# Optimization experiments

Measured on AMD Instinct MI355X. Metric: run time of the kernel, lower is better.

The kernel has to match this reference:

```python
import jax, jax.numpy as jnp
import numpy as np

N = 50000
E = 500000
D = 128
L = 3
BN_EPS = 1e-5


def setup_inputs() -> dict:
    key = jax.random.key(0)
    ks = jax.random.split(key, 16)

    def xavier(k, shape):
        fan_in, fan_out = shape[-2], shape[-1]
        limit = float(np.sqrt(6.0 / (fan_in + fan_out)))
        return jax.random.uniform(k, shape, jnp.float32, -limit, limit)

    inp = {
        "x": jax.random.randint(ks[0], (N, 2), 0, 3),
        "edge_index": jax.random.randint(ks[1], (2, E), 0, N),
        "edge_attr": jax.random.randint(ks[2], (E, 2), 0, 3),
        # atom embeddings (xavier_uniform like torch init)
        "atom_emb0": xavier(ks[3], (120, D)),
        "atom_emb1": xavier(ks[4], (3, D)),
        # per-layer edge embeddings, stacked over layers
        "edge_emb0": xavier(ks[5], (L, 5, D)),
        "edge_emb1": xavier(ks[6], (L, 3, D)),
        # per-layer MLP: Linear(D, 2D) -> ReLU -> Linear(2D, D)
        "W1": xavier(ks[7], (L, D, 2 * D)),
        "b1": jnp.zeros((L, 2 * D), jnp.float32),
        "W2": xavier(ks[8], (L, 2 * D, D)),
        "b2": jnp.zeros((L, D), jnp.float32),
        # batchnorm affine params
        "gamma": jnp.ones((L, D), jnp.float32),
        "beta": jnp.zeros((L, D), jnp.float32),
    }
    return inp


def reference(x, edge_index, edge_attr, atom_emb0, atom_emb1,
              edge_emb0, edge_emb1, W1, b1, W2, b2, gamma, beta):
    n = x.shape[0]
    num_layer = W1.shape[0]

    # atom embedding: sum of per-attribute embeddings -> [N, D]
    h = atom_emb0[x[:, 0]] + atom_emb1[x[:, 1]]

    # add self loops: src/dst both get arange(N) appended
    loop = jnp.arange(n, dtype=edge_index.dtype)
    src = jnp.concatenate([edge_index[0], loop])  # [E+N]
    dst = jnp.concatenate([edge_index[1], loop])  # [E+N]
    # self-loop edge attr is [4, 0]
    ea0 = jnp.concatenate([edge_attr[:, 0], jnp.full((n,), 4, edge_attr.dtype)])
    ea1 = jnp.concatenate([edge_attr[:, 1], jnp.zeros((n,), edge_attr.dtype)])

    for l in range(num_layer):
        # edge embedding lookup + message = x_j + edge_attr, scatter-add to dst
        eemb = edge_emb0[l][ea0] + edge_emb1[l][ea1]          # [E+N, D]
        msg = h[src] + eemb                                   # gather + add
        aggr = jax.ops.segment_sum(msg, dst, num_segments=n)  # [N, D]
        # MLP update
        hid = jax.nn.relu(aggr @ W1[l] + b1[l])               # [N, 2D]
        out = hid @ W2[l] + b2[l]                             # [N, D]
        # BatchNorm1d (training mode: batch stats, biased variance)
        mean = jnp.mean(out, axis=0)
        var = jnp.mean(jnp.square(out - mean), axis=0)
        out = gamma[l] * (out - mean) * jax.lax.rsqrt(var + BN_EPS) + beta[l]
        # dropout with p=0 is identity; ReLU on all but last layer
        h = out if l == num_layer - 1 else jax.nn.relu(out)
    return h
```

## Files before the change

kernel.cpp:

```cpp
#include <hip/hip_runtime.h>

#define D 128
#define TWO_D 256
#define BN_EPS 1e-5f

typedef __attribute__((ext_vector_type(8))) short bf16x8;
typedef __attribute__((ext_vector_type(4))) float f32x4;

__device__ __forceinline__ float relu_f(float x) { return x > 0.f ? x : 0.f; }

__device__ __forceinline__ unsigned short f2bf(float f) {
    unsigned u = __builtin_bit_cast(unsigned, f);
    return (unsigned short)((u + 0x7FFFu + ((u >> 16) & 1u)) >> 16);
}
__device__ __forceinline__ float bf2f(unsigned s) {
    unsigned u = s << 16;
    return __builtin_bit_cast(float, u);
}
__device__ __forceinline__ unsigned pack2(float a, float b) {
    return (unsigned)f2bf(a) | ((unsigned)f2bf(b) << 16);
}

__global__ void atom_embed_kernel(const int* __restrict__ x,
                                  const float* __restrict__ emb0,
                                  const float* __restrict__ emb1,
                                  unsigned short* __restrict__ hbf, int n) {
    int idx = blockIdx.x * blockDim.x + threadIdx.x;
    if (idx >= n * 32) return;
    int node = idx >> 5;
    int d0 = (idx & 31) << 2;
    int i0 = x[node * 2 + 0];
    int i1 = x[node * 2 + 1];
    const float4 a = *reinterpret_cast<const float4*>(emb0 + (size_t)i0 * D + d0);
    const float4 b = *reinterpret_cast<const float4*>(emb1 + (size_t)i1 * D + d0);
    uint2 v;
    v.x = pack2(a.x + b.x, a.y + b.y);
    v.y = pack2(a.z + b.z, a.w + b.w);
    *reinterpret_cast<uint2*>(hbf + (size_t)node * D + d0) = v;
}

__global__ void hist_kernel(const int* __restrict__ ei, int* __restrict__ counts, int e_cnt) {
    int e = blockIdx.x * blockDim.x + threadIdx.x;
    if (e >= e_cnt) return;
    atomicAdd(counts + ei[e_cnt + e], 1);
}

__global__ __launch_bounds__(256) void bsum_kernel(const int* __restrict__ counts,
                                                   int* __restrict__ bsum, int n) {
    __shared__ int s[256];
    int t = threadIdx.x;
    int idx = blockIdx.x * 256 + t;
    s[t] = (idx < n) ? counts[idx] : 0;
    __syncthreads();
    for (int off = 128; off > 0; off >>= 1) {
        if (t < off) s[t] += s[t + off];
        __syncthreads();
    }
    if (t == 0) bsum[blockIdx.x] = s[0];
}

__global__ __launch_bounds__(256) void bscan_kernel(const int* __restrict__ bsum,
                                                    int* __restrict__ bpre,
                                                    int* __restrict__ row_ptr, int nb, int n) {
    __shared__ int s[256];
    int t = threadIdx.x;
    s[t] = (t < nb) ? bsum[t] : 0;
    __syncthreads();
    for (int off = 1; off < 256; off <<= 1) {
        int v = (t >= off) ? s[t - off] : 0;
        __syncthreads();
        s[t] += v;
        __syncthreads();
    }
    bpre[t] = (t == 0) ? 0 : s[t - 1];
    if (t == 255) row_ptr[n] = s[255];
}

__global__ __launch_bounds__(256) void scan_apply_kernel(const int* __restrict__ counts,
                                                         const int* __restrict__ bpre,
                                                         int* __restrict__ row_ptr,
                                                         int* __restrict__ cursor, int n) {
    __shared__ int s[256];
    int t = threadIdx.x;
    int idx = blockIdx.x * 256 + t;
    int c = (idx < n) ? counts[idx] : 0;
    s[t] = c;
    __syncthreads();
    for (int off = 1; off < 256; off <<= 1) {
        int v = (t >= off) ? s[t - off] : 0;
        __syncthreads();
        s[t] += v;
        __syncthreads();
    }
    if (idx < n) {
        int excl = bpre[blockIdx.x] + s[t] - c;
        row_ptr[idx] = excl;
        cursor[idx] = excl;
    }
}

__global__ void fill_kernel(const int* __restrict__ ei, const int* __restrict__ ea,
                            int* __restrict__ cursor, int* __restrict__ epack, int e_cnt) {
    int e = blockIdx.x * blockDim.x + threadIdx.x;
    if (e >= e_cnt) return;
    int dst = ei[e_cnt + e];
    int src = ei[e];
    int aidx = ea[e * 2 + 0] * 3 + ea[e * 2 + 1];
    int pos = atomicAdd(cursor + dst, 1);
    epack[pos] = (src & 0x1FFFF) | (aidx << 17);
}

__global__ void frag_prep_kernel(const float* __restrict__ W1,
                                 const float* __restrict__ W2,
                                 unsigned short* __restrict__ w1f,
                                 unsigned short* __restrict__ w2f, int Lnum) {
    int tid = blockIdx.x * blockDim.x + threadIdx.x;
    if (tid >= Lnum * 128 * 64) return;
    int l = tid / 8192;
    int rem = tid % 8192;
    int frag = rem / 64;
    int lane = rem % 64;
    int kg = lane >> 4, cl = lane & 15;
    if (frag < 64) {
        int kk = frag >> 4, tn = frag & 15;
        const float* src = W1 + (size_t)l * D * TWO_D;
        int k0 = kk * 32 + kg * 8, col = tn * 16 + cl;
        unsigned short* dst = w1f + (size_t)l * 32768 + ((size_t)frag * 64 + lane) * 8;
        #pragma unroll
        for (int j = 0; j < 8; ++j) dst[j] = f2bf(src[(size_t)(k0 + j) * TWO_D + col]);
    } else {
        int f2 = frag - 64;
        int kk = f2 >> 3, tn = f2 & 7;
        const float* src = W2 + (size_t)l * TWO_D * D;
        int k0 = kk * 32 + kg * 8, col = tn * 16 + cl;
        unsigned short* dst = w2f + (size_t)l * 32768 + ((size_t)f2 * 64 + lane) * 8;
        #pragma unroll
        for (int j = 0; j < 8; ++j) dst[j] = f2bf(src[(size_t)(k0 + j) * D + col]);
    }
}

__global__ __launch_bounds__(256) void gather_kernel(
    const unsigned short* __restrict__ hbf,
    const float* __restrict__ ee0_l, const float* __restrict__ ee1_l,
    const float* __restrict__ scsh,
    const int* __restrict__ row_ptr, const int* __restrict__ epack,
    unsigned short* __restrict__ aggrbf, float* __restrict__ stats,
    int n, int do_bn) {

    __shared__ float cee[16 * D];
    const int t = threadIdx.x;
    if (blockIdx.x == 0) stats[t] = 0.f;
    for (int i = t; i < 16 * D; i += 256) {
        int r = i >> 7, d = i & 127;
        cee[i] = (r < 15) ? ee0_l[(r / 3) * D + d] + ee1_l[(r % 3) * D + d]
                          : ee0_l[4 * D + d] + ee1_l[d];
    }
    __syncthreads();
    int node = blockIdx.x * 8 + (t >> 5);
    if (node >= n) return;
    int d0 = (t & 31) << 2;

    const int jb = row_ptr[node];
    const int je = row_ptr[node + 1];
    float4 cs = *reinterpret_cast<const float4*>(cee + 15 * D + d0);
    float ax, ay, az, aw;

    if (do_bn) {
        const float4 sc = *reinterpret_cast<const float4*>(scsh + d0);
        const float4 sh = *reinterpret_cast<const float4*>(scsh + 128 + d0);
        uint2 hv = *reinterpret_cast<const uint2*>(hbf + (size_t)node * D + d0);
        ax = relu_f(bf2f(hv.x & 0xffffu) * sc.x + sh.x) + cs.x;
        ay = relu_f(bf2f(hv.x >> 16)     * sc.y + sh.y) + cs.y;
        az = relu_f(bf2f(hv.y & 0xffffu) * sc.z + sh.z) + cs.z;
        aw = relu_f(bf2f(hv.y >> 16)     * sc.w + sh.w) + cs.w;
        for (int j = jb; j < je; ++j) {
            int p = epack[j];
            int s = p & 0x1FFFF;
            int a = p >> 17;
            uint2 sv = *reinterpret_cast<const uint2*>(hbf + (size_t)s * D + d0);
            float4 ev = *reinterpret_cast<const float4*>(cee + a * D + d0);
            ax += relu_f(bf2f(sv.x & 0xffffu) * sc.x + sh.x) + ev.x;
            ay += relu_f(bf2f(sv.x >> 16)     * sc.y + sh.y) + ev.y;
            az += relu_f(bf2f(sv.y & 0xffffu) * sc.z + sh.z) + ev.z;
            aw += relu_f(bf2f(sv.y >> 16)     * sc.w + sh.w) + ev.w;
        }
    } else {
        uint2 hv = *reinterpret_cast<const uint2*>(hbf + (size_t)node * D + d0);
        ax = bf2f(hv.x & 0xffffu) + cs.x;
        ay = bf2f(hv.x >> 16)     + cs.y;
        az = bf2f(hv.y & 0xffffu) + cs.z;
        aw = bf2f(hv.y >> 16)     + cs.w;
        for (int j = jb; j < je; ++j) {
            int p = epack[j];
            int s = p & 0x1FFFF;
            int a = p >> 17;
            uint2 sv = *reinterpret_cast<const uint2*>(hbf + (size_t)s * D + d0);
            float4 ev = *reinterpret_cast<const float4*>(cee + a * D + d0);
            ax += bf2f(sv.x & 0xffffu) + ev.x;
            ay += bf2f(sv.x >> 16)     + ev.y;
            az += bf2f(sv.y & 0xffffu) + ev.z;
            aw += bf2f(sv.y >> 16)     + ev.w;
        }
    }
    uint2 o;
    o.x = pack2(ax, ay);
    o.y = pack2(az, aw);
    *reinterpret_cast<uint2*>(aggrbf + (size_t)node * D + d0) = o;
}

__global__ __launch_bounds__(256) void mlp_mfma_kernel(
    unsigned short* __restrict__ aggrbf,
    const bf16x8* __restrict__ w1f, const bf16x8* __restrict__ w2f,
    const float* __restrict__ b1l, const float* __restrict__ b2l,
    float* __restrict__ outf, float* __restrict__ stats, int n, int final_f32) {

    __shared__ unsigned short hid[16 * TWO_D];
    __shared__ float sred[256];

    const int wave = threadIdx.x >> 6;
    const int lane = threadIdx.x & 63;
    const int arow = lane & 15;
    const int kgrp = lane >> 4;

    bf16x8 W1[4][4];
    #pragma unroll
    for (int kk = 0; kk < 4; ++kk)
        #pragma unroll
        for (int t = 0; t < 4; ++t)
            W1[kk][t] = w1f[(kk * 16 + wave * 4 + t) * 64 + lane];
    bf16x8 W2[8][2];
    #pragma unroll
    for (int kk = 0; kk < 8; ++kk)
        #pragma unroll
        for (int t = 0; t < 2; ++t)
            W2[kk][t] = w2f[(kk * 8 + wave * 2 + t) * 64 + lane];

    float b1v[4], b2v[2];
    #pragma unroll
    for (int t = 0; t < 4; ++t) b1v[t] = b1l[wave * 64 + t * 16 + arow];
    #pragma unroll
    for (int t = 0; t < 2; ++t) b2v[t] = b2l[wave * 32 + t * 16 + arow];

    float ps[2] = {0.f, 0.f}, pq[2] = {0.f, 0.f};

    const int tiles = n >> 4;
    for (int tile = blockIdx.x; tile < tiles; tile += gridDim.x) {
        const size_t row0 = (size_t)tile * 16;

        bf16x8 a[4];
        #pragma unroll
        for (int kk = 0; kk < 4; ++kk)
            a[kk] = *reinterpret_cast<const bf16x8*>(
                aggrbf + (row0 + arow) * D + kk * 32 + kgrp * 8);

        f32x4 acc1[4];
        #pragma unroll
        for (int t = 0; t < 4; ++t) acc1[t] = (f32x4){0.f, 0.f, 0.f, 0.f};
        #pragma unroll
        for (int kk = 0; kk < 4; ++kk)
            #pragma unroll
            for (int t = 0; t < 4; ++t)
                acc1[t] = __builtin_amdgcn_mfma_f32_16x16x32_bf16(a[kk], W1[kk][t], acc1[t], 0, 0, 0);

        __syncthreads();
        #pragma unroll
        for (int t = 0; t < 4; ++t) {
            const int cc = wave * 64 + t * 16 + arow;
            #pragma unroll
            for (int r = 0; r < 4; ++r) {
                const int rr = kgrp * 4 + r;
                float v = relu_f(acc1[t][r] + b1v[t]);
                hid[(rr * TWO_D + cc) ^ ((rr & 7) << 3)] = f2bf(v);
            }
        }
        __syncthreads();

        f32x4 acc2[2];
        #pragma unroll
        for (int t = 0; t < 2; ++t) acc2[t] = (f32x4){0.f, 0.f, 0.f, 0.f};
        #pragma unroll
        for (int kk = 0; kk < 8; ++kk) {
            bf16x8 a2 = *reinterpret_cast<const bf16x8*>(
                hid + ((arow * TWO_D + kk * 32 + kgrp * 8) ^ ((arow & 7) << 3)));
            #pragma unroll
            for (int t = 0; t < 2; ++t)
                acc2[t] = __builtin_amdgcn_mfma_f32_16x16x32_bf16(a2, W2[kk][t], acc2[t], 0, 0, 0);
        }

        if (final_f32) {
            #pragma unroll
            for (int t = 0; t < 2; ++t) {
                const int col = wave * 32 + t * 16 + arow;
                #pragma unroll
                for (int r = 0; r < 4; ++r) {
                    float v = acc2[t][r] + b2v[t];
                    outf[(row0 + kgrp * 4 + r) * D + col] = v;
                    ps[t] += v; pq[t] += v * v;
                }
            }
        } else {
            #pragma unroll
            for (int t = 0; t < 2; ++t) {
                const int col = wave * 32 + t * 16 + arow;
                #pragma unroll
                for (int r = 0; r < 4; ++r) {
                    float v = acc2[t][r] + b2v[t];
                    aggrbf[(row0 + kgrp * 4 + r) * D + col] = f2bf(v);
                    ps[t] += v; pq[t] += v * v;
                }
            }
        }
    }

    sred[threadIdx.x] = 0.f;
    __syncthreads();
    #pragma unroll
    for (int t = 0; t < 2; ++t) {
        const int col = wave * 32 + t * 16 + arow;
        atomicAdd(sred + col, ps[t]);
        atomicAdd(sred + 128 + col, pq[t]);
    }
    __syncthreads();
    unsafeAtomicAdd(stats + threadIdx.x, sred[threadIdx.x]);
}

__global__ void bn_scale_kernel(const float* __restrict__ stats,
                                const float* __restrict__ gamma_l,
                                const float* __restrict__ beta_l,
                                float* __restrict__ scsh, float inv_n) {
    int c = threadIdx.x;
    float mean = stats[c] * inv_n;
    float var  = stats[128 + c] * inv_n - mean * mean;
    float sc = gamma_l[c] * rsqrtf(var + BN_EPS);
    scsh[c]       = sc;
    scsh[128 + c] = beta_l[c] - mean * sc;
}

__global__ void bn_apply_final_kernel(const float* __restrict__ out,
                                      const float* __restrict__ scsh,
                                      float* __restrict__ dst, int n) {
    int idx = blockIdx.x * blockDim.x + threadIdx.x;
    if (idx >= n * 32) return;
    int d0 = (idx & 31) << 2;
    float4 v  = *reinterpret_cast<const float4*>(out + (size_t)idx * 4);
    float4 sc = *reinterpret_cast<const float4*>(scsh + d0);
    float4 sh = *reinterpret_cast<const float4*>(scsh + 128 + d0);
    *reinterpret_cast<float4*>(dst + (size_t)idx * 4) =
        make_float4(v.x * sc.x + sh.x, v.y * sc.y + sh.y,
                    v.z * sc.z + sh.z, v.w * sc.w + sh.w);
}

extern "C" void kernel_launch(void* const* d_in, const int* in_sizes, int n_in,
                              void* d_out, int out_size, void* d_ws, size_t ws_size,
                              hipStream_t stream) {
    const int*   x     = (const int*)d_in[0];
    const int*   ei    = (const int*)d_in[1];
    const int*   ea    = (const int*)d_in[2];
    const float* aemb0 = (const float*)d_in[3];
    const float* aemb1 = (const float*)d_in[4];
    const float* eemb0 = (const float*)d_in[5];
    const float* eemb1 = (const float*)d_in[6];
    const float* W1    = (const float*)d_in[7];
    const float* b1    = (const float*)d_in[8];
    const float* W2    = (const float*)d_in[9];
    const float* b2    = (const float*)d_in[10];
    const float* gamma = (const float*)d_in[11];
    const float* beta  = (const float*)d_in[12];

    const int n = in_sizes[0] / 2;
    const int e = in_sizes[1] / 2;
    const int L = in_sizes[8] / TWO_D;

    char* ws = (char*)d_ws;
    float* outb = (float*)ws;                      ws += (size_t)n * D * 4;
    unsigned short* bufA = (unsigned short*)ws;    ws += (size_t)n * D * 2;
    unsigned short* bufB = (unsigned short*)ws;    ws += (size_t)n * D * 2;
    unsigned short* w1f = (unsigned short*)ws;     ws += (size_t)L * 32768 * 2;
    unsigned short* w2f = (unsigned short*)ws;     ws += (size_t)L * 32768 * 2;
    float* stats = (float*)ws;                     ws += 256 * 4;
    float* scsh  = (float*)ws;                     ws += 256 * 4;
    int* counts  = (int*)ws;                       ws += (size_t)n * 4;
    int* row_ptr = (int*)ws;                       ws += (size_t)(n + 1) * 4;
    int* cursor  = (int*)ws;                       ws += (size_t)n * 4;
    int* bsum    = (int*)ws;                       ws += 256 * 4;
    int* bpre    = (int*)ws;                       ws += 256 * 4;
    int* epack   = (int*)ws;

    const int edge_blocks = (e + 255) / 256;
    const int vec_blocks  = (n * 32 + 255) / 256;
    const int node_blocks = (n + 7) / 8;
    const int nb = (n + 255) / 256;

    hipMemsetAsync(counts, 0, (size_t)n * sizeof(int), stream);
    hist_kernel<<<edge_blocks, 256, 0, stream>>>(ei, counts, e);
    bsum_kernel<<<nb, 256, 0, stream>>>(counts, bsum, n);
    bscan_kernel<<<1, 256, 0, stream>>>(bsum, bpre, row_ptr, nb, n);
    scan_apply_kernel<<<nb, 256, 0, stream>>>(counts, bpre, row_ptr, cursor, n);
    fill_kernel<<<edge_blocks, 256, 0, stream>>>(ei, ea, cursor, epack, e);
    frag_prep_kernel<<<(L * 128 * 64 + 255) / 256, 256, 0, stream>>>(W1, W2, w1f, w2f, L);
    atom_embed_kernel<<<vec_blocks, 256, 0, stream>>>(x, aemb0, aemb1, bufA, n);

    for (int l = 0; l < L; ++l) {
        const float* ee0_l = eemb0 + (size_t)l * 5 * D;
        const float* ee1_l = eemb1 + (size_t)l * 3 * D;
        const float* b1l   = b1 + (size_t)l * TWO_D;
        const float* b2l   = b2 + (size_t)l * D;

        unsigned short* src = (l & 1) ? bufB : bufA;
        unsigned short* dst = (l & 1) ? bufA : bufB;

        gather_kernel<<<node_blocks, 256, 0, stream>>>(src, ee0_l, ee1_l, scsh,
                                                       row_ptr, epack, dst, stats,
                                                       n, (l > 0) ? 1 : 0);
        mlp_mfma_kernel<<<512, 256, 0, stream>>>(
            dst,
            (const bf16x8*)(w1f + (size_t)l * 32768),
            (const bf16x8*)(w2f + (size_t)l * 32768),
            b1l, b2l, outb, stats, n, (l == L - 1) ? 1 : 0);
        bn_scale_kernel<<<1, D, 0, stream>>>(stats, gamma + (size_t)l * D, beta + (size_t)l * D,
                                             scsh, 1.0f / (float)n);
    }
    bn_apply_final_kernel<<<vec_blocks, 256, 0, stream>>>(outb, scsh, (float*)d_out, n);
}
```

Before: 316.6 us.

## Fold BN scale into consumers, batch edge gathers, count edge-attr embeddings, pair MLP tiles

The per-layer bn_scale kernel is removed. Each gather block and the final apply kernel now recompute the BN scale and shift from the stats, using double-buffered stats arrays. The gather loop is unrolled by 8 to keep more row loads in flight, and it counts how many edges use each edge-attribute type so the embedding sums are added once per node as count*embedding instead of once per edge. The MLP kernel processes two 16-row tiles per iteration to amortize barriers, at the cost of more registers and shared memory. The packed 8-bit counters could overflow if a node has 256 or more edges of one type.

```diff
diff --git a/kernel.cpp b/kernel.cpp
--- a/kernel.cpp
+++ b/kernel.cpp
@@ -139,73 +139,120 @@
     }
 }
 
+template<int DO_BN>
 __global__ __launch_bounds__(256) void gather_kernel(
     const unsigned short* __restrict__ hbf,
     const float* __restrict__ ee0_l, const float* __restrict__ ee1_l,
-    const float* __restrict__ scsh,
+    const float* __restrict__ stats_prev,
+    const float* __restrict__ gamma_p, const float* __restrict__ beta_p,
+    float inv_n,
     const int* __restrict__ row_ptr, const int* __restrict__ epack,
-    unsigned short* __restrict__ aggrbf, float* __restrict__ stats,
-    int n, int do_bn) {
+    unsigned short* __restrict__ aggrbf, float* __restrict__ stats_cur, int n) {
 
     __shared__ float cee[16 * D];
+    __shared__ float sbn[2 * D];
     const int t = threadIdx.x;
-    if (blockIdx.x == 0) stats[t] = 0.f;
+    if (blockIdx.x == 0) stats_cur[t] = 0.f;
     for (int i = t; i < 16 * D; i += 256) {
         int r = i >> 7, d = i & 127;
         cee[i] = (r < 15) ? ee0_l[(r / 3) * D + d] + ee1_l[(r % 3) * D + d]
                           : ee0_l[4 * D + d] + ee1_l[d];
     }
-    __syncthreads();
+    if (DO_BN && t < 128) {
+        float mean = stats_prev[t] * inv_n;
+        float var  = stats_prev[128 + t] * inv_n - mean * mean;
+        float sc = gamma_p[t] * rsqrtf(var + BN_EPS);
+        sbn[t] = sc;
+        sbn[128 + t] = beta_p[t] - mean * sc;
+    }
+    __syncthreads();
+
     int node = blockIdx.x * 8 + (t >> 5);
     if (node >= n) return;
     int d0 = (t & 31) << 2;
 
+    float4 sc = make_float4(1.f, 1.f, 1.f, 1.f);
+    float4 sh = make_float4(0.f, 0.f, 0.f, 0.f);
+    if (DO_BN) {
+        sc = *reinterpret_cast<const float4*>(sbn + d0);
+        sh = *reinterpret_cast<const float4*>(sbn + 128 + d0);
+    }
+
     const int jb = row_ptr[node];
     const int je = row_ptr[node + 1];
-    float4 cs = *reinterpret_cast<const float4*>(cee + 15 * D + d0);
+
     float ax, ay, az, aw;
-
-    if (do_bn) {
-        const float4 sc = *reinterpret_cast<const float4*>(scsh + d0);
-        const float4 sh = *reinterpret_cast<const float4*>(scsh + 128 + d0);
+    {
+        const float4 cs = *reinterpret_cast<const float4*>(cee + 15 * D + d0);
         uint2 hv = *reinterpret_cast<const uint2*>(hbf + (size_t)node * D + d0);
-        ax = relu_f(bf2f(hv.x & 0xffffu) * sc.x + sh.x) + cs.x;
-        ay = relu_f(bf2f(hv.x >> 16)     * sc.y + sh.y) + cs.y;
-        az = relu_f(bf2f(hv.y & 0xffffu) * sc.z + sh.z) + cs.z;
-        aw = relu_f(bf2f(hv.y >> 16)     * sc.w + sh.w) + cs.w;
-        for (int j = jb; j < je; ++j) {
-            int p = epack[j];
-            int s = p & 0x1FFFF;
-            int a = p >> 17;
-            uint2 sv = *reinterpret_cast<const uint2*>(hbf + (size_t)s * D + d0);
-            float4 ev = *reinterpret_cast<const float4*>(cee + a * D + d0);
-            ax += relu_f(bf2f(sv.x & 0xffffu) * sc.x + sh.x) + ev.x;
-            ay += relu_f(bf2f(sv.x >> 16)     * sc.y + sh.y) + ev.y;
-            az += relu_f(bf2f(sv.y & 0xffffu) * sc.z + sh.z) + ev.z;
-            aw += relu_f(bf2f(sv.y >> 16)     * sc.w + sh.w) + ev.w;
+        if (DO_BN) {
+            ax = relu_f(bf2f(hv.x & 0xffffu) * sc.x + sh.x) + cs.x;
+            ay = relu_f(bf2f(hv.x >> 16)     * sc.y + sh.y) + cs.y;
+            az = relu_f(bf2f(hv.y & 0xffffu) * sc.z + sh.z) + cs.z;
+            aw = relu_f(bf2f(hv.y >> 16)     * sc.w + sh.w) + cs.w;
+        } else {
+            ax = bf2f(hv.x & 0xffffu) + cs.x;
+            ay = bf2f(hv.x >> 16)     + cs.y;
+            az = bf2f(hv.y & 0xffffu) + cs.z;
+            aw = bf2f(hv.y >> 16)     + cs.w;
         }
-    } else {
-        uint2 hv = *reinterpret_cast<const uint2*>(hbf + (size_t)node * D + d0);
-        ax = bf2f(hv.x & 0xffffu) + cs.x;
-        ay = bf2f(hv.x >> 16)     + cs.y;
-        az = bf2f(hv.y & 0xffffu) + cs.z;
-        aw = bf2f(hv.y >> 16)     + cs.w;
-        for (int j = jb; j < je; ++j) {
-            int p = epack[j];
-            int s = p & 0x1FFFF;
-            int a = p >> 17;
-            uint2 sv = *reinterpret_cast<const uint2*>(hbf + (size_t)s * D + d0);
-            float4 ev = *reinterpret_cast<const float4*>(cee + a * D + d0);
-            ax += bf2f(sv.x & 0xffffu) + ev.x;
-            ay += bf2f(sv.x >> 16)     + ev.y;
-            az += bf2f(sv.y & 0xffffu) + ev.z;
-            aw += bf2f(sv.y >> 16)     + ev.w;
-        }
-    }
+    }
+
+    unsigned long long c0 = 0ull;
+    int cnt8 = 0;
+
+#define ROWLD(p) (*reinterpret_cast<const uint2*>(hbf + (size_t)((p) & 0x1FFFF) * D + d0))
+#define CNTUPD(p) do { int a_ = (p) >> 17; \
+        unsigned long long bit_ = 1ull << ((a_ & 7) << 3); \
+        c0 += (a_ < 8) ? bit_ : 0ull; cnt8 += (a_ >> 3); } while (0)
+#define EACC(sv) do { \
+        if (DO_BN) { \
+            ax += relu_f(bf2f((sv).x & 0xffffu) * sc.x + sh.x); \
+            ay += relu_f(bf2f((sv).x >> 16)     * sc.y + sh.y); \
+            az += relu_f(bf2f((sv).y & 0xffffu) * sc.z + sh.z); \
+            aw += relu_f(bf2f((sv).y >> 16)     * sc.w + sh.w); \
+        } else { \
+            ax += bf2f((sv).x & 0xffffu); ay += bf2f((sv).x >> 16); \
+            az += bf2f((sv).y & 0xffffu); aw += bf2f((sv).y >> 16); \
+        } } while (0)
+
+    int j = jb;
+    for (; j + 8 <= je; j += 8) {
+        const int p0 = epack[j + 0], p1 = epack[j + 1], p2 = epack[j + 2], p3 = epack[j + 3];
+        const int p4 = epack[j + 4], p5 = epack[j + 5], p6 = epack[j + 6], p7 = epack[j + 7];
+        const uint2 s0 = ROWLD(p0), s1 = ROWLD(p1), s2 = ROWLD(p2), s3 = ROWLD(p3);
+        const uint2 s4 = ROWLD(p4), s5 = ROWLD(p5), s6 = ROWLD(p6), s7 = ROWLD(p7);
+        CNTUPD(p0); CNTUPD(p1); CNTUPD(p2); CNTUPD(p3);
+        CNTUPD(p4); CNTUPD(p5); CNTUPD(p6); CNTUPD(p7);
+        EACC(s0); EACC(s1); EACC(s2); EACC(s3);
+        EACC(s4); EACC(s5); EACC(s6); EACC(s7);
+    }
+    for (; j < je; ++j) {
+        const int p = epack[j];
+        const uint2 sv = ROWLD(p);
+        CNTUPD(p);
+        EACC(sv);
+    }
+
+    #pragma unroll
+    for (int a = 0; a < 8; ++a) {
+        float fc = (float)((unsigned)(c0 >> (a * 8)) & 0xFFu);
+        const float4 ev = *reinterpret_cast<const float4*>(cee + a * D + d0);
+        ax += fc * ev.x; ay += fc * ev.y; az += fc * ev.z; aw += fc * ev.w;
+    }
+    {
+        float fc = (float)cnt8;
+        const float4 ev = *reinterpret_cast<const float4*>(cee + 8 * D + d0);
+        ax += fc * ev.x; ay += fc * ev.y; az += fc * ev.z; aw += fc * ev.w;
+    }
+
     uint2 o;
     o.x = pack2(ax, ay);
     o.y = pack2(az, aw);
     *reinterpret_cast<uint2*>(aggrbf + (size_t)node * D + d0) = o;
+#undef ROWLD
+#undef CNTUPD
+#undef EACC
 }
 
 __global__ __launch_bounds__(256) void mlp_mfma_kernel(
@@ -214,7 +261,7 @@
     const float* __restrict__ b1l, const float* __restrict__ b2l,
     float* __restrict__ outf, float* __restrict__ stats, int n, int final_f32) {
 
-    __shared__ unsigned short hid[16 * TWO_D];
+    __shared__ unsigned short hid[32 * TWO_D];
     __shared__ float sred[256];
 
     const int wave = threadIdx.x >> 6;
@@ -244,14 +291,23 @@
     float ps[2] = {0.f, 0.f}, pq[2] = {0.f, 0.f};
 
     const int tiles = n >> 4;
-    for (int tile = blockIdx.x; tile < tiles; tile += gridDim.x) {
-        const size_t row0 = (size_t)tile * 16;
-
-        bf16x8 a[4];
+    const int npair = (tiles + 1) >> 1;
+    for (int p = blockIdx.x; p < npair; p += gridDim.x) {
+        const int t0i = 2 * p, t1i = 2 * p + 1;
+        const bool has1 = (t1i < tiles);
+        const size_t r0 = (size_t)t0i * 16, r1 = (size_t)t1i * 16;
+
+        bf16x8 a0[4], a1[4];
         #pragma unroll
         for (int kk = 0; kk < 4; ++kk)
-            a[kk] = *reinterpret_cast<const bf16x8*>(
-                aggrbf + (row0 + arow) * D + kk * 32 + kgrp * 8);
+            a0[kk] = *reinterpret_cast<const bf16x8*>(
+                aggrbf + (r0 + arow) * D + kk * 32 + kgrp * 8);
+        if (has1) {
+            #pragma unroll
+            for (int kk = 0; kk < 4; ++kk)
+                a1[kk] = *reinterpret_cast<const bf16x8*>(
+                    aggrbf + (r1 + arow) * D + kk * 32 + kgrp * 8);
+        }
 
         f32x4 acc1[4];
         #pragma unroll
@@ -260,7 +316,7 @@
         for (int kk = 0; kk < 4; ++kk)
             #pragma unroll
             for (int t = 0; t < 4; ++t)
-                acc1[t] = __builtin_amdgcn_mfma_f32_16x16x32_bf16(a[kk], W1[kk][t], acc1[t], 0, 0, 0);
+                acc1[t] = __builtin_amdgcn_mfma_f32_16x16x32_bf16(a0[kk], W1[kk][t], acc1[t], 0, 0, 0);
 
         __syncthreads();
         #pragma unroll
@@ -269,43 +325,74 @@
             #pragma unroll
             for (int r = 0; r < 4; ++r) {
                 const int rr = kgrp * 4 + r;
-                float v = relu_f(acc1[t][r] + b1v[t]);
-                hid[(rr * TWO_D + cc) ^ ((rr & 7) << 3)] = f2bf(v);
+                hid[(rr * TWO_D + cc) ^ ((rr & 7) << 3)] = f2bf(relu_f(acc1[t][r] + b1v[t]));
             }
         }
-        __syncthreads();
-
-        f32x4 acc2[2];
-        #pragma unroll
-        for (int t = 0; t < 2; ++t) acc2[t] = (f32x4){0.f, 0.f, 0.f, 0.f};
-        #pragma unroll
-        for (int kk = 0; kk < 8; ++kk) {
-            bf16x8 a2 = *reinterpret_cast<const bf16x8*>(
-                hid + ((arow * TWO_D + kk * 32 + kgrp * 8) ^ ((arow & 7) << 3)));
-            #pragma unroll
-            for (int t = 0; t < 2; ++t)
-                acc2[t] = __builtin_amdgcn_mfma_f32_16x16x32_bf16(a2, W2[kk][t], acc2[t], 0, 0, 0);
+
+        if (has1) {
+            #pragma unroll
+            for (int t = 0; t < 4; ++t) acc1[t] = (f32x4){0.f, 0.f, 0.f, 0.f};
+            #pragma unroll
+            for (int kk = 0; kk < 4; ++kk)
+                #pragma unroll
+                for (int t = 0; t < 4; ++t)
+                    acc1[t] = __builtin_amdgcn_mfma_f32_16x16x32_bf16(a1[kk], W1[kk][t], acc1[t], 0, 0, 0);
+            #pragma unroll
+            for (int t = 0; t < 4; ++t) {
+                const int cc = wave * 64 + t * 16 + arow;
+                #pragma unroll
+                for (int r = 0; r < 4; ++r) {
+                    const int rr = 16 + kgrp * 4 + r;
+                    hid[(rr * TWO_D + cc) ^ ((rr & 7) << 3)] = f2bf(relu_f(acc1[t][r] + b1v[t]));
+                }
+            }
         }
-
-        if (final_f32) {
+        __syncthreads();
+
+        {
+            f32x4 acc2[2];
+            #pragma unroll
+            for (int t = 0; t < 2; ++t) acc2[t] = (f32x4){0.f, 0.f, 0.f, 0.f};
+            #pragma unroll
+            for (int kk = 0; kk < 8; ++kk) {
+                bf16x8 a2 = *reinterpret_cast<const bf16x8*>(
+                    hid + ((arow * TWO_D + kk * 32 + kgrp * 8) ^ ((arow & 7) << 3)));
+                #pragma unroll
+                for (int t = 0; t < 2; ++t)
+                    acc2[t] = __builtin_amdgcn_mfma_f32_16x16x32_bf16(a2, W2[kk][t], acc2[t], 0, 0, 0);
+            }
             #pragma unroll
             for (int t = 0; t < 2; ++t) {
                 const int col = wave * 32 + t * 16 + arow;
                 #pragma unroll
                 for (int r = 0; r < 4; ++r) {
                     float v = acc2[t][r] + b2v[t];
-                    outf[(row0 + kgrp * 4 + r) * D + col] = v;
+                    if (final_f32) outf[(r0 + kgrp * 4 + r) * D + col] = v;
+                    else           aggrbf[(r0 + kgrp * 4 + r) * D + col] = f2bf(v);
                     ps[t] += v; pq[t] += v * v;
                 }
             }
-        } else {
+        }
+        if (has1) {
+            f32x4 acc2[2];
+            #pragma unroll
+            for (int t = 0; t < 2; ++t) acc2[t] = (f32x4){0.f, 0.f, 0.f, 0.f};
+            #pragma unroll
+            for (int kk = 0; kk < 8; ++kk) {
+                bf16x8 a2 = *reinterpret_cast<const bf16x8*>(
+                    hid + (((16 + arow) * TWO_D + kk * 32 + kgrp * 8) ^ ((arow & 7) << 3)));
+                #pragma unroll
+                for (int t = 0; t < 2; ++t)
+                    acc2[t] = __builtin_amdgcn_mfma_f32_16x16x32_bf16(a2, W2[kk][t], acc2[t], 0, 0, 0);
+            }
             #pragma unroll
             for (int t = 0; t < 2; ++t) {
                 const int col = wave * 32 + t * 16 + arow;
                 #pragma unroll
                 for (int r = 0; r < 4; ++r) {
                     float v = acc2[t][r] + b2v[t];
-                    aggrbf[(row0 + kgrp * 4 + r) * D + col] = f2bf(v);
+                    if (final_f32) outf[(r1 + kgrp * 4 + r) * D + col] = v;
+                    else           aggrbf[(r1 + kgrp * 4 + r) * D + col] = f2bf(v);
                     ps[t] += v; pq[t] += v * v;
                 }
             }
@@ -324,27 +411,28 @@
     unsafeAtomicAdd(stats + threadIdx.x, sred[threadIdx.x]);
 }
 
-__global__ void bn_scale_kernel(const float* __restrict__ stats,
-                                const float* __restrict__ gamma_l,
-                                const float* __restrict__ beta_l,
-                                float* __restrict__ scsh, float inv_n) {
-    int c = threadIdx.x;
-    float mean = stats[c] * inv_n;
-    float var  = stats[128 + c] * inv_n - mean * mean;
-    float sc = gamma_l[c] * rsqrtf(var + BN_EPS);
-    scsh[c]       = sc;
-    scsh[128 + c] = beta_l[c] - mean * sc;
-}
-
 __global__ void bn_apply_final_kernel(const float* __restrict__ out,
-                                      const float* __restrict__ scsh,
+                                      const float* __restrict__ stats,
+                                      const float* __restrict__ gamma_l,
+                                      const float* __restrict__ beta_l,
+                                      float inv_n,
                                       float* __restrict__ dst, int n) {
-    int idx = blockIdx.x * blockDim.x + threadIdx.x;
+    __shared__ float sbn[2 * D];
+    int t = threadIdx.x;
+    if (t < 128) {
+        float mean = stats[t] * inv_n;
+        float var  = stats[128 + t] * inv_n - mean * mean;
+        float sc = gamma_l[t] * rsqrtf(var + BN_EPS);
+        sbn[t] = sc;
+        sbn[128 + t] = beta_l[t] - mean * sc;
+    }
+    __syncthreads();
+    int idx = blockIdx.x * blockDim.x + t;
     if (idx >= n * 32) return;
     int d0 = (idx & 31) << 2;
     float4 v  = *reinterpret_cast<const float4*>(out + (size_t)idx * 4);
-    float4 sc = *reinterpret_cast<const float4*>(scsh + d0);
-    float4 sh = *reinterpret_cast<const float4*>(scsh + 128 + d0);
+    float4 sc = *reinterpret_cast<const float4*>(sbn + d0);
+    float4 sh = *reinterpret_cast<const float4*>(sbn + 128 + d0);
     *reinterpret_cast<float4*>(dst + (size_t)idx * 4) =
         make_float4(v.x * sc.x + sh.x, v.y * sc.y + sh.y,
                     v.z * sc.z + sh.z, v.w * sc.w + sh.w);
@@ -370,6 +458,7 @@
     const int n = in_sizes[0] / 2;
     const int e = in_sizes[1] / 2;
     const int L = in_sizes[8] / TWO_D;
+    const float inv_n = 1.0f / (float)n;
 
     char* ws = (char*)d_ws;
     float* outb = (float*)ws;                      ws += (size_t)n * D * 4;
@@ -377,8 +466,8 @@
     unsigned short* bufB = (unsigned short*)ws;    ws += (size_t)n * D * 2;
     unsigned short* w1f = (unsigned short*)ws;     ws += (size_t)L * 32768 * 2;
     unsigned short* w2f = (unsigned short*)ws;     ws += (size_t)L * 32768 * 2;
-    float* stats = (float*)ws;                     ws += 256 * 4;
-    float* scsh  = (float*)ws;                     ws += 256 * 4;
+    float* statsA = (float*)ws;                    ws += 256 * 4;
+    float* statsB = (float*)ws;                    ws += 256 * 4;
     int* counts  = (int*)ws;                       ws += (size_t)n * 4;
     int* row_ptr = (int*)ws;                       ws += (size_t)(n + 1) * 4;
     int* cursor  = (int*)ws;                       ws += (size_t)n * 4;
@@ -408,17 +497,28 @@
 
         unsigned short* src = (l & 1) ? bufB : bufA;
         unsigned short* dst = (l & 1) ? bufA : bufB;
-
-        gather_kernel<<<node_blocks, 256, 0, stream>>>(src, ee0_l, ee1_l, scsh,
-                                                       row_ptr, epack, dst, stats,
-                                                       n, (l > 0) ? 1 : 0);
+        float* stats_cur  = (l & 1) ? statsB : statsA;
+        float* stats_prev = (l & 1) ? statsA : statsB;
+
+        if (l == 0)
+            gather_kernel<0><<<node_blocks, 256, 0, stream>>>(
+                src, ee0_l, ee1_l, nullptr, nullptr, nullptr, inv_n,
+                row_ptr, epack, dst, stats_cur, n);
+        else
+            gather_kernel<1><<<node_blocks, 256, 0, stream>>>(
+                src, ee0_l, ee1_l, stats_prev,
+                gamma + (size_t)(l - 1) * D, beta + (size_t)(l - 1) * D, inv_n,
+                row_ptr, epack, dst, stats_cur, n);
+
         mlp_mfma_kernel<<<512, 256, 0, stream>>>(
             dst,
             (const bf16x8*)(w1f + (size_t)l * 32768),
             (const bf16x8*)(w2f + (size_t)l * 32768),
-            b1l, b2l, outb, stats, n, (l == L - 1) ? 1 : 0);
-        bn_scale_kernel<<<1, D, 0, stream>>>(stats, gamma + (size_t)l * D, beta + (size_t)l * D,
-                                             scsh, 1.0f / (float)n);
-    }
-    bn_apply_final_kernel<<<vec_blocks, 256, 0, stream>>>(outb, scsh, (float*)d_out, n);
-}
+            b1l, b2l, outb, stats_cur, n, (l == L - 1) ? 1 : 0);
+    }
+
+    float* stats_last = ((L - 1) & 1) ? statsB : statsA;
+    bn_apply_final_kernel<<<vec_blocks, 256, 0, stream>>>(
+        outb, stats_last, gamma + (size_t)(L - 1) * D, beta + (size_t)(L - 1) * D,
+        inv_n, (float*)d_out, n);
+}
```

Result: faster. 278.8 us (-12.0%).
